# Optimization experiments

Measured on AMD Instinct MI355X. Metric: run time of the kernel, lower is better.

Reference implementation:

```python
import jax, jax.numpy as jnp
import numpy as np
from jax import lax

N = 8192  # total_nodes


def setup_inputs() -> dict:
    key = jax.random.key(0)
    kx, kW = jax.random.split(key)
    x = jax.random.normal(kx, (2,), dtype=jnp.float32)
    W = jax.random.normal(kW, (N, N), dtype=jnp.float32) * 0.1
    b = jnp.zeros((N,), dtype=jnp.float32)
    return {"x": x, "W": W, "b": b}


def reference(x, W, b):
    # Sequential DAG scan: s[j] = sigmoid(sum_{i<j} W[i,j] * s[i] + b[j])
    # (triu mask with diagonal=1 is all-ones over the slice [:j, j])
    n = W.shape[0]
    idx = jnp.arange(n)
    s0 = jnp.zeros((n,), dtype=W.dtype).at[0].set(x[0]).at[1].set(x[1])

    def step(s, j):
        m = (idx < j).astype(s.dtype)          # strict-upper-triangular mask column
        ws = jnp.sum(W[:, j] * m * s)          # weighted sum over predecessors
        val = jax.nn.sigmoid(ws + b[j])
        return s.at[j].set(val), None

    s, _ = lax.scan(step, s0, jnp.arange(2, n))
    return s[n - 1]
```

## Files before the change

### kernel.cpp

```cpp
#include <hip/hip_runtime.h>

#define NN 8192
#define SBS 512
#define NSB 16
#define LOG2E 1.44269504088896f

#define FR(k,w) (32 + ((k)*8 + (w))*32)
#define PART_OFF 8192
#define CP_OFF   16384
#define NCPROW   9
#define SARR_OFF (CP_OFF + NCPROW * NN)

__device__ __forceinline__ float bcastf(float v, int lane) {
    return __int_as_float(__builtin_amdgcn_readlane(__float_as_int(v), lane));
}
__device__ __forceinline__ float sigm(float prelog) {
    return __builtin_amdgcn_rcpf(1.0f + __builtin_amdgcn_exp2f(-prelog));
}
__device__ __forceinline__ int ld_flag(const int* p) {
    return __hip_atomic_load(p, __ATOMIC_RELAXED, __HIP_MEMORY_SCOPE_AGENT);
}
__device__ __forceinline__ void st_rel(int* p, int v) {
    __hip_atomic_store(p, v, __ATOMIC_RELEASE, __HIP_MEMORY_SCOPE_AGENT);
}
__device__ __forceinline__ float ldf(const float* p) {
    return __hip_atomic_load(p, __ATOMIC_RELAXED, __HIP_MEMORY_SCOPE_AGENT);
}
__device__ __forceinline__ void stf(float* p, float v) {
    __hip_atomic_store(p, v, __ATOMIC_RELAXED, __HIP_MEMORY_SCOPE_AGENT);
}
#define LBAR() do { asm volatile("s_waitcnt lgkmcnt(0)\ns_barrier" ::: "memory"); \
                    __builtin_amdgcn_sched_barrier(0); } while (0)

__global__ void init_ws(int* wsi, float* wsf) {
    int i = blockIdx.x * 256 + threadIdx.x;
    if (i < 8192) wsi[i] = 0;
    wsf[CP_OFF + i] = 0.0f;
}

__device__ void solver_fn(const float* __restrict__ W, const float* __restrict__ b,
                          const float* __restrict__ x, float* wsf, int* flags,
                          float* sdiag, float* spub, float* sacc,
                          float (*redN)[8][64], float (*redF)[8][64],
                          float* __restrict__ out, int k) {
    const int tid = threadIdx.x;
    const int w = tid >> 6, l = tid & 63;
    const int dj = tid >> 3, dc = (tid & 7) * 8;
    const int J0 = k * SBS;
    const float* cp = wsf + CP_OFF;
    float* partials = wsf + PART_OFF;
    float* s_arr = wsf + SARR_OFF;

    auto load_diag = [&](int mm, float4& a, float4& bq) {
        const float* p = &W[(size_t)(J0 + mm*64 + dj) * NN + (J0 + mm*64 + dc)];
        a  = *(const float4*)p;
        bq = *(const float4*)(p + 4);
    };
    auto write_diag = [&](int mm, float4 a, float4 bq) {
        float* dst = &sdiag[mm*4096 + dj*64 + dc];
        float v[8] = {a.x, a.y, a.z, a.w, bq.x, bq.y, bq.z, bq.w};
        #pragma unroll
        for (int e = 0; e < 8; ++e) dst[e] = (dj < dc + e) ? v[e] * LOG2E : 0.0f;
    };
    auto load_pan1 = [&](int mm, float* pr) {
        #pragma unroll
        for (int r = 0; r < 8; ++r)
            pr[r] = W[(size_t)(J0 + mm*64 + w*8 + r) * NN + (J0 + (mm+1)*64 + l)];
    };
    auto load_pan2 = [&](int mm, float* pr) {
        #pragma unroll
        for (int r = 0; r < 8; ++r)
            pr[r] = W[(size_t)(J0 + mm*64 + w*8 + r) * NN + (J0 + (mm+2)*64 + l)];
    };

    const float x0 = x[0], x1 = x[1];
    float base = b[J0 + tid];
    #pragma unroll
    for (int r = 0; r < NCPROW; ++r) base += cp[r * NN + J0 + tid];
    float4 dA[2], dB[2];
    load_diag(0, dA[0], dB[0]);
    load_diag(1, dA[1], dB[1]);
    float p1[2][8], p2[2][8];
    load_pan1(0, p1[0]);
    load_pan1(1, p1[1]);
    load_pan2(0, p2[0]);
    load_pan2(1, p2[1]);
    write_diag(0, dA[0], dB[0]);
    write_diag(1, dA[1], dB[1]);
    sacc[tid] = base;
    redF[1][w][l] = 0.0f;
    LBAR();

    #pragma unroll
    for (int m = 0; m < 8; ++m) {
        if (w == m) {
            float part = 0.0f;
            if (m >= 3) {
                const int* fl = &flags[FR(k, m)];
                while (ld_flag(fl) == 0) {}
                __builtin_amdgcn_fence(__ATOMIC_ACQUIRE, "agent");
                part = ldf(&partials[((size_t)k*8 + m)*64 + l]);
            }
            float rsum = 0.0f;
            if (m >= 1) {
                #pragma unroll
                for (int g = 0; g < 8; ++g) rsum += redN[m & 1][g][l];
            }
            if (m >= 2) {
                #pragma unroll
                for (int g = 0; g < 8; ++g) rsum += redF[m & 1][g][l];
            }
            float acc = (sacc[m*64 + l] + rsum + part) * LOG2E;
            float smine = 0.0f;
            const bool first = (k == 0) && (m == 0);
            #pragma unroll
            for (int j = 0; j < 64; ++j) {
                const float pre = bcastf(acc, j);
                float s;
                if (first && j == 0)      s = x0;
                else if (first && j == 1) s = x1;
                else                      s = sigm(pre);
                acc += sdiag[m*4096 + j*64 + l] * s;
                if (l == j) smine = s;
            }
            spub[m*64 + l] = smine;
            stf(&s_arr[J0 + m*64 + l], smine);
            if (k == NSB - 1 && m == 7 && l == 63) out[0] = smine;
            if (l == 0) st_rel(&flags[0], k*8 + m + 1);
        }
        LBAR();
        if (m < 7) {
            float f1 = 0.0f;
            #pragma unroll
            for (int r = 0; r < 8; ++r)
                f1 += p1[m & 1][r] * spub[m*64 + w*8 + r];
            redN[(m+1) & 1][w][l] = f1;
            if (m < 6) {
                float f2 = 0.0f;
                #pragma unroll
                for (int r = 0; r < 8; ++r)
                    f2 += p2[m & 1][r] * spub[m*64 + w*8 + r];
                redF[m & 1][w][l] = f2;
            }
            if (m >= 1) write_diag(m + 1, dA[(m+1) & 1], dB[(m+1) & 1]);
            if (m + 2 <= 7) load_diag(m + 2, dA[(m+2) & 1], dB[(m+2) & 1]);
            if (m + 2 <= 6) load_pan1(m + 2, p1[m & 1]);
            if (m + 2 <= 5) load_pan2(m + 2, p2[m & 1]);
            LBAR();
        }
    }
}

template <int TW>
__device__ void helper_fn(const float* __restrict__ W, float* wsf, int* flags,
                          float (*redh)[64], int k) {
    const int tid = threadIdx.x, g = tid >> 6, l = tid & 63;
    float* partials = wsf + PART_OFF;
    const float* s_arr = wsf + SARR_OFF;
    const int J0 = k * SBS;

    float pr[TW - 2][8];
    #pragma unroll
    for (int m = 0; m <= TW - 3; ++m)
        #pragma unroll
        for (int r = 0; r < 8; ++r)
            pr[m][r] = W[(size_t)(J0 + m*64 + g*8 + r) * NN + (J0 + TW*64 + l)];

    float part = 0.0f;
    #pragma unroll
    for (int m = 0; m <= TW - 3; ++m) {
        if (tid < 64) {
            while (ld_flag(&flags[0]) < k*8 + m + 1) __builtin_amdgcn_s_sleep(2);
        }
        __syncthreads();
        __builtin_amdgcn_fence(__ATOMIC_ACQUIRE, "agent");
        #pragma unroll
        for (int r = 0; r < 8; ++r)
            part += pr[m][r] * ldf(&s_arr[J0 + m*64 + g*8 + r]);
    }
    redh[g][l] = part;
    __syncthreads();
    if (tid < 64) {
        float tot = 0.0f;
        #pragma unroll
        for (int g2 = 0; g2 < 8; ++g2) tot += redh[g2][tid];
        stf(&partials[((size_t)k*8 + TW)*64 + tid], tot);
    }
    __syncthreads();
    if (tid == 0) st_rel(&flags[FR(k, TW)], 1);
}

__device__ void near_fn(const float* __restrict__ W, float* wsf, int* flags,
                        float (*redh)[64], int t, int k) {
    const int tid = threadIdx.x, g = tid >> 6, l = tid & 63;
    const int col = (k+1)*SBS + t*64 + l;
    const float* s_arr = wsf + SARR_OFF;
    float* cp = wsf + CP_OFF;

    float pr[8][8];
    #pragma unroll
    for (int m = 0; m < 8; ++m)
        #pragma unroll
        for (int r = 0; r < 8; ++r)
            pr[m][r] = W[(size_t)(k*SBS + m*64 + g*8 + r) * NN + col];

    float part = 0.0f;
    #pragma unroll
    for (int m = 0; m < 8; ++m) {
        if (tid < 64) {
            while (ld_flag(&flags[0]) < k*8 + m + 1) __builtin_amdgcn_s_sleep(4);
        }
        __syncthreads();
        __builtin_amdgcn_fence(__ATOMIC_ACQUIRE, "agent");
        #pragma unroll
        for (int r = 0; r < 8; ++r)
            part += pr[m][r] * ldf(&s_arr[k*SBS + m*64 + g*8 + r]);
    }
    redh[g][l] = part;
    __syncthreads();
    if (g == 0) {
        float tot = 0.0f;
        #pragma unroll
        for (int g2 = 0; g2 < 8; ++g2) tot += redh[g2][l];
        cp[8 * NN + col] = tot;
    }
}

__device__ void bulk_fn(const float* __restrict__ W, float* wsf,
                        float* ssh, int idx, int k) {
    const int tid = threadIdx.x;
    const int rc = idx & 7, cg = idx >> 3;
    const int row0 = (k-1)*SBS + rc*64;
    const int col = (k+1)*SBS + cg*SBS + tid;
    const float* s_arr = wsf + SARR_OFF;
    float* cp = wsf + CP_OFF;

    if (tid < 64) ssh[tid] = s_arr[row0 + tid];
    __syncthreads();
    const float* wp = W + (size_t)row0 * NN + col;
    float a0 = 0.f, a1 = 0.f, a2 = 0.f, a3 = 0.f;
    #pragma unroll
    for (int i = 0; i < 64; i += 4) {
        a0 += wp[(size_t)(i + 0) * NN] * ssh[i + 0];
        a1 += wp[(size_t)(i + 1) * NN] * ssh[i + 1];
        a2 += wp[(size_t)(i + 2) * NN] * ssh[i + 2];
        a3 += wp[(size_t)(i + 3) * NN] * ssh[i + 3];
    }
    cp[rc * NN + col] += (a0 + a1) + (a2 + a3);
}

__global__ void __launch_bounds__(512, 1) mega_kernel(
    const float* __restrict__ W, const float* __restrict__ b,
    const float* __restrict__ x, float* wsf, int* flags,
    float* __restrict__ out, int k)
{
    __shared__ float sdiag[8 * 4096];
    __shared__ float spub[512];
    __shared__ float sacc[512];
    __shared__ float redN[2][8][64];
    __shared__ float redF[2][8][64];
    __shared__ float redh[8][64];
    const int bid = blockIdx.x;
    if (bid == 0) {
        solver_fn(W, b, x, wsf, flags, sdiag, spub, sacc, redN, redF, out, k);
    } else if (bid <= 5) {
        switch (bid) {
            case 1: helper_fn<3>(W, wsf, flags, redh, k); break;
            case 2: helper_fn<4>(W, wsf, flags, redh, k); break;
            case 3: helper_fn<5>(W, wsf, flags, redh, k); break;
            case 4: helper_fn<6>(W, wsf, flags, redh, k); break;
            case 5: helper_fn<7>(W, wsf, flags, redh, k); break;
        }
    } else if (bid <= 13) {
        near_fn(W, wsf, flags, redh, bid - 6, k);
    } else {
        bulk_fn(W, wsf, &redh[0][0], bid - 14, k);
    }
}

extern "C" void kernel_launch(void* const* d_in, const int* in_sizes, int n_in,
                              void* d_out, int out_size, void* d_ws, size_t ws_size,
                              hipStream_t stream) {
    const float* x = (const float*)d_in[0];
    const float* W = (const float*)d_in[1];
    const float* b = (const float*)d_in[2];
    float* out = (float*)d_out;
    float* wsf = (float*)d_ws;
    int* wsi   = (int*)d_ws;

    init_ws<<<dim3(288), dim3(256), 0, stream>>>(wsi, wsf);
    for (int k = 0; k < NSB; ++k) {
        int nb;
        if (k == 0)            nb = 14;
        else if (k == NSB - 1) nb = 6;
        else                   nb = 14 + (15 - k) * 8;
        mega_kernel<<<dim3(nb), dim3(512), 0, stream>>>(W, b, x, wsf, wsi, out, k);
    }
}
```

Measured before the change: 411.7 us.

## Offload far-panel reduction to helpers, spread blocks across XCDs, prefetch next diagonal

The solver block no longer computes the two-tiles-ahead panel product (redF). A new helper_fn<2> block computes that contribution and publishes it through the partials/flag path, so the solver waits on a helper flag from tile 2 onward. Helper blocks move to block ids that are multiples of 8, and a new block 56 reads the next superblock's diagonal and near-panel tiles. The intent is for those blocks to land on the same XCD as the solver under round-robin scheduling, warming its L2 before the next launch. Diag loads that would be fully masked are skipped and helper polling sleeps less. In exchange, more blocks are launched (including idle ones for late k), and the solver now depends on cross-block flag latency for tile 2.

```diff
diff --git a/kernel.cpp b/kernel.cpp
--- a/kernel.cpp
+++ b/kernel.cpp
@@ -41,8 +41,7 @@
 __device__ void solver_fn(const float* __restrict__ W, const float* __restrict__ b,
                           const float* __restrict__ x, float* wsf, int* flags,
                           float* sdiag, float* spub, float* sacc,
-                          float (*redN)[8][64], float (*redF)[8][64],
-                          float* __restrict__ out, int k) {
+                          float (*redN)[8][64], float* __restrict__ out, int k) {
     const int tid = threadIdx.x;
     const int w = tid >> 6, l = tid & 63;
     const int dj = tid >> 3, dc = (tid & 7) * 8;
@@ -52,9 +51,13 @@
     float* s_arr = wsf + SARR_OFF;
 
     auto load_diag = [&](int mm, float4& a, float4& bq) {
-        const float* p = &W[(size_t)(J0 + mm*64 + dj) * NN + (J0 + mm*64 + dc)];
-        a  = *(const float4*)p;
-        bq = *(const float4*)(p + 4);
+        if (dj < dc + 7) {
+            const float* p = &W[(size_t)(J0 + mm*64 + dj) * NN + (J0 + mm*64 + dc)];
+            a  = *(const float4*)p;
+            bq = *(const float4*)(p + 4);
+        } else {
+            a = make_float4(0.f,0.f,0.f,0.f); bq = make_float4(0.f,0.f,0.f,0.f);
+        }
     };
     auto write_diag = [&](int mm, float4 a, float4 bq) {
         float* dst = &sdiag[mm*4096 + dj*64 + dc];
@@ -67,11 +70,6 @@
         for (int r = 0; r < 8; ++r)
             pr[r] = W[(size_t)(J0 + mm*64 + w*8 + r) * NN + (J0 + (mm+1)*64 + l)];
     };
-    auto load_pan2 = [&](int mm, float* pr) {
-        #pragma unroll
-        for (int r = 0; r < 8; ++r)
-            pr[r] = W[(size_t)(J0 + mm*64 + w*8 + r) * NN + (J0 + (mm+2)*64 + l)];
-    };
 
     const float x0 = x[0], x1 = x[1];
     float base = b[J0 + tid];
@@ -80,22 +78,19 @@
     float4 dA[2], dB[2];
     load_diag(0, dA[0], dB[0]);
     load_diag(1, dA[1], dB[1]);
-    float p1[2][8], p2[2][8];
+    float p1[2][8];
     load_pan1(0, p1[0]);
     load_pan1(1, p1[1]);
-    load_pan2(0, p2[0]);
-    load_pan2(1, p2[1]);
     write_diag(0, dA[0], dB[0]);
     write_diag(1, dA[1], dB[1]);
     sacc[tid] = base;
-    redF[1][w][l] = 0.0f;
     LBAR();
 
     #pragma unroll
     for (int m = 0; m < 8; ++m) {
         if (w == m) {
             float part = 0.0f;
-            if (m >= 3) {
+            if (m >= 2) {
                 const int* fl = &flags[FR(k, m)];
                 while (ld_flag(fl) == 0) {}
                 __builtin_amdgcn_fence(__ATOMIC_ACQUIRE, "agent");
@@ -105,10 +100,6 @@
             if (m >= 1) {
                 #pragma unroll
                 for (int g = 0; g < 8; ++g) rsum += redN[m & 1][g][l];
-            }
-            if (m >= 2) {
-                #pragma unroll
-                for (int g = 0; g < 8; ++g) rsum += redF[m & 1][g][l];
             }
             float acc = (sacc[m*64 + l] + rsum + part) * LOG2E;
             float smine = 0.0f;
@@ -135,17 +126,9 @@
             for (int r = 0; r < 8; ++r)
                 f1 += p1[m & 1][r] * spub[m*64 + w*8 + r];
             redN[(m+1) & 1][w][l] = f1;
-            if (m < 6) {
-                float f2 = 0.0f;
-                #pragma unroll
-                for (int r = 0; r < 8; ++r)
-                    f2 += p2[m & 1][r] * spub[m*64 + w*8 + r];
-                redF[m & 1][w][l] = f2;
-            }
             if (m >= 1) write_diag(m + 1, dA[(m+1) & 1], dB[(m+1) & 1]);
             if (m + 2 <= 7) load_diag(m + 2, dA[(m+2) & 1], dB[(m+2) & 1]);
             if (m + 2 <= 6) load_pan1(m + 2, p1[m & 1]);
-            if (m + 2 <= 5) load_pan2(m + 2, p2[m & 1]);
             LBAR();
         }
     }
@@ -159,18 +142,18 @@
     const float* s_arr = wsf + SARR_OFF;
     const int J0 = k * SBS;
 
-    float pr[TW - 2][8];
-    #pragma unroll
-    for (int m = 0; m <= TW - 3; ++m)
+    float pr[TW - 1][8];
+    #pragma unroll
+    for (int m = 0; m <= TW - 2; ++m)
         #pragma unroll
         for (int r = 0; r < 8; ++r)
             pr[m][r] = W[(size_t)(J0 + m*64 + g*8 + r) * NN + (J0 + TW*64 + l)];
 
     float part = 0.0f;
     #pragma unroll
-    for (int m = 0; m <= TW - 3; ++m) {
+    for (int m = 0; m <= TW - 2; ++m) {
         if (tid < 64) {
-            while (ld_flag(&flags[0]) < k*8 + m + 1) __builtin_amdgcn_s_sleep(2);
+            while (ld_flag(&flags[0]) < k*8 + m + 1) __builtin_amdgcn_s_sleep(1);
         }
         __syncthreads();
         __builtin_amdgcn_fence(__ATOMIC_ACQUIRE, "agent");
@@ -188,6 +171,28 @@
     }
     __syncthreads();
     if (tid == 0) st_rel(&flags[FR(k, TW)], 1);
+}
+
+__device__ void prefetch_fn(const float* __restrict__ W, int k) {
+    const int tid = threadIdx.x;
+    const int w = tid >> 6, l = tid & 63;
+    const int dj = tid >> 3, dc = (tid & 7) * 8;
+    const int J0 = (k + 1) * SBS;
+    float s = 0.0f;
+    #pragma unroll
+    for (int mm = 0; mm < 8; ++mm) {
+        if (dj < dc + 7) {
+            const float* p = &W[(size_t)(J0 + mm*64 + dj) * NN + (J0 + mm*64 + dc)];
+            float4 a = *(const float4*)p, bq = *(const float4*)(p + 4);
+            s += (a.x + a.y) + (a.z + a.w) + (bq.x + bq.y) + (bq.z + bq.w);
+        }
+    }
+    #pragma unroll
+    for (int mm = 0; mm < 7; ++mm)
+        #pragma unroll
+        for (int r = 0; r < 8; ++r)
+            s += W[(size_t)(J0 + mm*64 + w*8 + r) * NN + (J0 + (mm+1)*64 + l)];
+    asm volatile("" :: "v"(s));
 }
 
 __device__ void near_fn(const float* __restrict__ W, float* wsf, int* flags,
@@ -258,23 +263,35 @@
     __shared__ float spub[512];
     __shared__ float sacc[512];
     __shared__ float redN[2][8][64];
-    __shared__ float redF[2][8][64];
     __shared__ float redh[8][64];
     const int bid = blockIdx.x;
     if (bid == 0) {
-        solver_fn(W, b, x, wsf, flags, sdiag, spub, sacc, redN, redF, out, k);
-    } else if (bid <= 5) {
-        switch (bid) {
-            case 1: helper_fn<3>(W, wsf, flags, redh, k); break;
-            case 2: helper_fn<4>(W, wsf, flags, redh, k); break;
-            case 3: helper_fn<5>(W, wsf, flags, redh, k); break;
-            case 4: helper_fn<6>(W, wsf, flags, redh, k); break;
-            case 5: helper_fn<7>(W, wsf, flags, redh, k); break;
-        }
-    } else if (bid <= 13) {
-        near_fn(W, wsf, flags, redh, bid - 6, k);
-    } else {
-        bulk_fn(W, wsf, &redh[0][0], bid - 14, k);
+        solver_fn(W, b, x, wsf, flags, sdiag, spub, sacc, redN, out, k);
+        return;
+    }
+    if ((bid & 7) == 0 && bid <= 48) {
+        switch (bid >> 3) {
+            case 1: helper_fn<2>(W, wsf, flags, redh, k); break;
+            case 2: helper_fn<3>(W, wsf, flags, redh, k); break;
+            case 3: helper_fn<4>(W, wsf, flags, redh, k); break;
+            case 4: helper_fn<5>(W, wsf, flags, redh, k); break;
+            case 5: helper_fn<6>(W, wsf, flags, redh, k); break;
+            case 6: helper_fn<7>(W, wsf, flags, redh, k); break;
+        }
+        return;
+    }
+    if (bid == 56) {
+        if (k < NSB - 1) prefetch_fn(W, k);
+        return;
+    }
+    if (bid < 10) {
+        if (k < NSB - 1) near_fn(W, wsf, flags, redh, (bid < 8) ? bid - 1 : 7, k);
+        return;
+    }
+    if (k >= 1) {
+        int nh = (bid >> 3) - 1; if (nh > 6) nh = 6;
+        int idx = bid - 10 - nh;
+        if (idx < 8 * (15 - k)) bulk_fn(W, wsf, &redh[0][0], idx, k);
     }
 }
 
@@ -291,9 +308,10 @@
     init_ws<<<dim3(288), dim3(256), 0, stream>>>(wsi, wsf);
     for (int k = 0; k < NSB; ++k) {
         int nb;
-        if (k == 0)            nb = 14;
-        else if (k == NSB - 1) nb = 6;
-        else                   nb = 14 + (15 - k) * 8;
+        if (k == 0)            nb = 57;
+        else if (k == NSB - 1) nb = 49;
+        else if (k <= 9)       nb = 8 * (15 - k) + 16;
+        else                   nb = 57;
         mega_kernel<<<dim3(nb), dim3(512), 0, stream>>>(W, b, x, wsf, wsi, out, k);
     }
 }
```

New measurement: 449.0 us. 9.1% more time.
